# Kernel optimization log

Measured on AMD Instinct MI355X. Metric: run time of the kernel, lower is better.

Reference implementation:

```python
import jax, jax.numpy as jnp
import numpy as np

B, S, D, H, F = 8, 1024, 768, 12, 3072
DH = D // H
C_QUAD = 5.0
LN_EPS = 1e-5


def layer_norm(x, g, b):
    mu = jnp.mean(x, axis=-1, keepdims=True)
    var = jnp.mean(jnp.square(x - mu), axis=-1, keepdims=True)
    return (x - mu) * jax.lax.rsqrt(var + LN_EPS) * g + b


def setup_inputs() -> dict:
    key = jax.random.key(0)
    ks = jax.random.split(key, 8)
    s_in = 1.0 / np.sqrt(D)
    s_ff = 1.0 / np.sqrt(F)
    return {
        "x": jax.random.normal(ks[0], (B, S, D), jnp.float32),
        "wqkv": jax.random.normal(ks[1], (D, 3 * D), jnp.float32) * s_in,
        "bqkv": jnp.zeros((3 * D,), jnp.float32),
        "wo": jax.random.normal(ks[2], (D, D), jnp.float32) * s_in,
        "bo": jnp.zeros((D,), jnp.float32),
        "ln1_g": jnp.ones((D,), jnp.float32),
        "ln1_b": jnp.zeros((D,), jnp.float32),
        "w1": jax.random.normal(ks[3], (D, F), jnp.float32) * s_in,
        "b1": jnp.zeros((F,), jnp.float32),
        "w2": jax.random.normal(ks[4], (F, D), jnp.float32) * s_ff,
        "b2": jnp.zeros((D,), jnp.float32),
        "ln2_g": jnp.ones((D,), jnp.float32),
        "ln2_b": jnp.zeros((D,), jnp.float32),
    }


def quad2(scores):
    # Quad2 custom 'softmax': (s + c)^2 normalized by row sum
    s2 = jnp.square(scores + C_QUAD)
    return s2 / jnp.sum(s2, axis=-1, keepdims=True)


def reference(x, wqkv, bqkv, wo, bo, ln1_g, ln1_b, w1, b1, w2, b2, ln2_g, ln2_b):
    # --- pre-norm multi-head attention with Quad2 score normalization ---
    h = layer_norm(x, ln1_g, ln1_b)
    qkv = h @ wqkv + bqkv                              # [B,S,3D]
    q, k, v = jnp.split(qkv, 3, axis=-1)
    q = q.reshape(B, S, H, DH).transpose(0, 2, 1, 3)   # [B,H,S,Dh]
    k = k.reshape(B, S, H, DH).transpose(0, 2, 1, 3)
    v = v.reshape(B, S, H, DH).transpose(0, 2, 1, 3)
    scale = 1.0 / np.sqrt(DH)
    scores = jnp.einsum("bhqd,bhkd->bhqk", q, k) * scale
    attn = quad2(scores)                               # [B,H,S,S]
    ctx = jnp.einsum("bhqk,bhkd->bhqd", attn, v)
    ctx = ctx.transpose(0, 2, 1, 3).reshape(B, S, D)
    x = x + ctx @ wo + bo
    # --- pre-norm FFN ---
    h = layer_norm(x, ln2_g, ln2_b)
    h = jax.nn.gelu(h @ w1 + b1)
    x = x + h @ w2 + b2
    return x
```

## Files before the change

kernel.cpp:

```cpp
#include <hip/hip_runtime.h>
#include <hip/hip_bf16.h>

constexpr int B_ = 8;
constexpr int S_ = 1024;
constexpr int D_ = 768;
constexpr int H_ = 12;
constexpr int F_ = 3072;
constexpr int DH_ = 64;
constexpr int M_ = B_ * S_;
constexpr int PSZ = B_ * S_ * D_;

typedef __bf16 bf16x8 __attribute__((ext_vector_type(8)));
typedef float f32x4 __attribute__((ext_vector_type(4)));
typedef short s16x8 __attribute__((ext_vector_type(8)));
typedef short s16x4 __attribute__((ext_vector_type(4)));

__device__ __forceinline__ void gload_lds16(const __bf16* g, __bf16* l) {
    __builtin_amdgcn_global_load_lds(
        (const __attribute__((address_space(1))) void*)g,
        (__attribute__((address_space(3))) void*)l,
        16, 0, 0);
}

__device__ __forceinline__ float fast_gelu(float x) {
    float z = 0.7978845608028654f * (x + 0.044715f * x * x * x);
    z = fminf(fmaxf(z, -15.0f), 15.0f);
    float e = __builtin_amdgcn_exp2f(2.8853900817779268f * z);
    float th = (e - 1.0f) / (e + 1.0f);
    return 0.5f * x * (1.0f + th);
}

__global__ __launch_bounds__(256) void transpose_cvt(const float* __restrict__ in,
                                                     __bf16* __restrict__ out,
                                                     int K, int N) {
    __shared__ float t[32][33];
    int tx = threadIdx.x, ty = threadIdx.y;
    int n0 = blockIdx.x * 32, k0 = blockIdx.y * 32;
#pragma unroll
    for (int i = 0; i < 4; ++i)
        t[ty + i * 8][tx] = in[(size_t)(k0 + ty + i * 8) * N + n0 + tx];
    __syncthreads();
#pragma unroll
    for (int i = 0; i < 4; ++i)
        out[(size_t)(n0 + ty + i * 8) * K + k0 + tx] = (__bf16)t[tx][ty + i * 8];
}

__global__ __launch_bounds__(256) void ln_kernel(const float* __restrict__ x,
                                                 const float* __restrict__ g,
                                                 const float* __restrict__ bb,
                                                 __bf16* __restrict__ out) {
    int row = blockIdx.x;
    const float* xr = x + (size_t)row * D_;
    int tid = threadIdx.x;
    float v[3];
    float s = 0.f, s2 = 0.f;
#pragma unroll
    for (int j = 0; j < 3; ++j) {
        v[j] = xr[tid + j * 256];
        s += v[j];
        s2 += v[j] * v[j];
    }
#pragma unroll
    for (int o = 32; o >= 1; o >>= 1) {
        s += __shfl_xor(s, o, 64);
        s2 += __shfl_xor(s2, o, 64);
    }
    __shared__ float red[8];
    int wid = tid >> 6, lane = tid & 63;
    if (lane == 0) { red[wid] = s; red[4 + wid] = s2; }
    __syncthreads();
    s = red[0] + red[1] + red[2] + red[3];
    s2 = red[4] + red[5] + red[6] + red[7];
    float mu = s * (1.0f / D_);
    float var = s2 * (1.0f / D_) - mu * mu;
    float rs = rsqrtf(var + 1e-5f);
    __bf16* orow = out + (size_t)row * D_;
#pragma unroll
    for (int j = 0; j < 3; ++j) {
        int i = tid + j * 256;
        orow[i] = (__bf16)((v[j] - mu) * rs * g[i] + bb[i]);
    }
}

template <int EPI>
__global__ __launch_bounds__(256) void gemm4(const __bf16* __restrict__ A,
                                             const __bf16* __restrict__ Bt,
                                             const float* __restrict__ bias,
                                             const float* __restrict__ res,
                                             float* __restrict__ outf,
                                             __bf16* __restrict__ outb,
                                             int M, int N, int K) {
    constexpr int BK = 64;
    __shared__ __bf16 lds[2][256 * BK];

    const int tid = threadIdx.x;
    const int lane = tid & 63, wid = tid >> 6;
    const int wm = wid >> 1, wn = wid & 1;
    const int bm = blockIdx.y * 128, bn = blockIdx.x * 128;
    const int l15 = lane & 15, l4 = lane >> 4;
    f32x4 acc[4][4] = {};

    const int r8 = tid >> 3;
    const int swc = ((tid & 7) ^ (r8 & 7)) * 8;
    const __bf16* ga = A + (size_t)(bm + r8) * K + swc;
    const __bf16* gb = Bt + (size_t)(bn + r8) * K + swc;
    const int NT = K / BK;

    auto stage = [&](int t, int s) {
        const int kt = t * BK;
        __bf16* base = &lds[s][0] + tid * 8;
#pragma unroll
        for (int j = 0; j < 4; ++j)
            gload_lds16(ga + kt + (size_t)j * 32 * K, base + j * 2048);
#pragma unroll
        for (int j = 0; j < 4; ++j)
            gload_lds16(gb + kt + (size_t)j * 32 * K, base + 8192 + j * 2048);
    };

    auto compute = [&](int s) {
        const __bf16* sA = &lds[s][0];
        const __bf16* sB = &lds[s][0] + 8192;
        const int swr = (l15 & 7) * 8;
        bf16x8 a[4][2], b[4][2];
#pragma unroll
        for (int mf = 0; mf < 4; ++mf) {
            int row = wm * 64 + mf * 16 + l15;
#pragma unroll
            for (int ks = 0; ks < 2; ++ks)
                a[mf][ks] = *(const bf16x8*)&sA[row * 64 + ((ks * 32 + l4 * 8) ^ swr)];
        }
#pragma unroll
        for (int nf = 0; nf < 4; ++nf) {
            int row = wn * 64 + nf * 16 + l15;
#pragma unroll
            for (int ks = 0; ks < 2; ++ks)
                b[nf][ks] = *(const bf16x8*)&sB[row * 64 + ((ks * 32 + l4 * 8) ^ swr)];
        }
        __builtin_amdgcn_s_setprio(1);
#pragma unroll
        for (int ks = 0; ks < 2; ++ks)
#pragma unroll
            for (int mf = 0; mf < 4; ++mf)
#pragma unroll
                for (int nf = 0; nf < 4; ++nf)
                    acc[mf][nf] = __builtin_amdgcn_mfma_f32_16x16x32_bf16(
                        a[mf][ks], b[nf][ks], acc[mf][nf], 0, 0, 0);
        __builtin_amdgcn_s_setprio(0);
    };

    stage(0, 0);
    for (int t = 0; t < NT; ++t) {
        if (t + 1 < NT) {
            stage(t + 1, (t + 1) & 1);
            asm volatile("s_waitcnt vmcnt(8)" ::: "memory");
        } else {
            asm volatile("s_waitcnt vmcnt(0)" ::: "memory");
        }
        asm volatile("s_barrier" ::: "memory");
        compute(t & 1);
        asm volatile("s_barrier" ::: "memory");
    }

#pragma unroll
    for (int mf = 0; mf < 4; ++mf) {
#pragma unroll
        for (int nf = 0; nf < 4; ++nf) {
#pragma unroll
            for (int r = 0; r < 4; ++r) {
                int m = bm + wm * 64 + mf * 16 + l4 * 4 + r;
                int n = bn + wn * 64 + nf * 16 + l15;
                float val = acc[mf][nf][r] + bias[n];
                if constexpr (EPI == 0) {
                    int part = n / 768;
                    int n7 = n - part * 768;
                    int head = n7 >> 6, dh = n7 & 63;
                    int bI = m >> 10, sI = m & 1023;
                    outb[(size_t)part * PSZ +
                         (((size_t)bI * H_ + head) * S_ + sI) * DH_ + dh] = (__bf16)val;
                } else if constexpr (EPI == 1) {
                    outf[(size_t)m * N + n] = val + res[(size_t)m * N + n];
                } else {
                    outb[(size_t)m * N + n] = (__bf16)fast_gelu(val);
                }
            }
        }
    }
}

__global__ __launch_bounds__(256) void attn_kernel(const __bf16* __restrict__ qg,
                                                   const __bf16* __restrict__ kg,
                                                   const __bf16* __restrict__ vg,
                                                   __bf16* __restrict__ ctx) {
    __shared__ __bf16 Ks[64][72];
    __shared__ __bf16 Vt[64][72];
    __shared__ __bf16 Pw[4][32][72];
    __shared__ float den_l[4][32];
    int tid = threadIdx.x, lane = tid & 63, wid = tid >> 6;
    int l15 = lane & 15, l4 = lane >> 4;
    int bh = blockIdx.x >> 3, qt = blockIdx.x & 7;
    int q0 = qt * 128;
    const __bf16* qbase = qg + (size_t)bh * S_ * DH_;
    const __bf16* kbase = kg + (size_t)bh * S_ * DH_;
    const __bf16* vbase = vg + (size_t)bh * S_ * DH_;

    int wq0 = q0 + wid * 32;
    bf16x8 qf[2][2];
#pragma unroll
    for (int qi = 0; qi < 2; ++qi)
#pragma unroll
        for (int ks = 0; ks < 2; ++ks)
            qf[qi][ks] = *(const bf16x8*)(qbase + (size_t)(wq0 + qi * 16 + l15) * DH_ +
                                          ks * 32 + l4 * 8);

    f32x4 oacc[2][4] = {};
    float den[2] = {0.f, 0.f};
    const float scale = 0.125f;

    for (int k0 = 0; k0 < S_; k0 += 64) {
        {
            int key = tid >> 2, dc = (tid & 3) * 16;
            *(s16x8*)&Ks[key][dc] =
                *(const s16x8*)(kbase + (size_t)(k0 + key) * DH_ + dc);
            *(s16x8*)&Ks[key][dc + 8] =
                *(const s16x8*)(kbase + (size_t)(k0 + key) * DH_ + dc + 8);
            int vkey = tid & 63, dg = (tid >> 6) * 16;
            s16x8 v0 = *(const s16x8*)(vbase + (size_t)(k0 + vkey) * DH_ + dg);
            s16x8 v1 = *(const s16x8*)(vbase + (size_t)(k0 + vkey) * DH_ + dg + 8);
#pragma unroll
            for (int e = 0; e < 8; ++e) {
                Vt[dg + e][vkey] = ((const __bf16*)&v0)[e];
                Vt[dg + 8 + e][vkey] = ((const __bf16*)&v1)[e];
            }
        }
        __syncthreads();

        bf16x8 kf[4][2];
#pragma unroll
        for (int kfi = 0; kfi < 4; ++kfi)
#pragma unroll
            for (int ks = 0; ks < 2; ++ks)
                kf[kfi][ks] = *(const bf16x8*)&Ks[kfi * 16 + l15][ks * 32 + l4 * 8];

#pragma unroll
        for (int qi = 0; qi < 2; ++qi) {
#pragma unroll
            for (int kfi = 0; kfi < 4; ++kfi) {
                f32x4 sa = {};
                sa = __builtin_amdgcn_mfma_f32_16x16x32_bf16(kf[kfi][0], qf[qi][0], sa, 0, 0, 0);
                sa = __builtin_amdgcn_mfma_f32_16x16x32_bf16(kf[kfi][1], qf[qi][1], sa, 0, 0, 0);
                __bf16 pk[4];
#pragma unroll
                for (int r = 0; r < 4; ++r) {
                    float p = sa[r] * scale + 5.0f;
                    p = p * p;
                    den[qi] += p;
                    pk[r] = (__bf16)p;
                }
                *(s16x4*)&Pw[wid][qi * 16 + l15][kfi * 16 + l4 * 4] =
                    *(const s16x4*)pk;
            }
        }

#pragma unroll
        for (int mf = 0; mf < 2; ++mf) {
#pragma unroll
            for (int ks = 0; ks < 2; ++ks) {
                bf16x8 pa = *(const bf16x8*)&Pw[wid][mf * 16 + l15][ks * 32 + l4 * 8];
#pragma unroll
                for (int nf = 0; nf < 4; ++nf) {
                    bf16x8 vb = *(const bf16x8*)&Vt[nf * 16 + l15][ks * 32 + l4 * 8];
                    oacc[mf][nf] = __builtin_amdgcn_mfma_f32_16x16x32_bf16(
                        pa, vb, oacc[mf][nf], 0, 0, 0);
                }
            }
        }
        __syncthreads();
    }

#pragma unroll
    for (int qi = 0; qi < 2; ++qi) {
        den[qi] += __shfl_xor(den[qi], 16, 64);
        den[qi] += __shfl_xor(den[qi], 32, 64);
    }
    if (lane < 16) {
        den_l[wid][lane] = den[0];
        den_l[wid][16 + lane] = den[1];
    }
    __syncthreads();

    int b_ = bh / H_, h_ = bh - b_ * H_;
#pragma unroll
    for (int mf = 0; mf < 2; ++mf)
#pragma unroll
        for (int nf = 0; nf < 4; ++nf)
#pragma unroll
            for (int r = 0; r < 4; ++r) {
                int qrow = mf * 16 + l4 * 4 + r;
                int dcol = nf * 16 + l15;
                float val = oacc[mf][nf][r] / den_l[wid][qrow];
                int sI = q0 + wid * 32 + qrow;
                ctx[((size_t)b_ * S_ + sI) * D_ + h_ * DH_ + dcol] = (__bf16)val;
            }
}

extern "C" void kernel_launch(void* const* d_in, const int* in_sizes, int n_in,
                              void* d_out, int out_size, void* d_ws, size_t ws_size,
                              hipStream_t stream) {
    const float* x    = (const float*)d_in[0];
    const float* wqkv = (const float*)d_in[1];
    const float* bqkv = (const float*)d_in[2];
    const float* wo   = (const float*)d_in[3];
    const float* bo   = (const float*)d_in[4];
    const float* ln1g = (const float*)d_in[5];
    const float* ln1b = (const float*)d_in[6];
    const float* w1   = (const float*)d_in[7];
    const float* b1   = (const float*)d_in[8];
    const float* w2   = (const float*)d_in[9];
    const float* b2   = (const float*)d_in[10];
    const float* ln2g = (const float*)d_in[11];
    const float* ln2b = (const float*)d_in[12];
    float* out = (float*)d_out;

    char* ws = (char*)d_ws;
    size_t off = 0;
    auto alloc = [&](size_t bytes) {
        void* p = ws + off;
        off += (bytes + 255) & ~(size_t)255;
        return p;
    };
    __bf16* wqkvT = (__bf16*)alloc((size_t)(3 * D_) * D_ * 2);
    __bf16* woT   = (__bf16*)alloc((size_t)D_ * D_ * 2);
    __bf16* w1T   = (__bf16*)alloc((size_t)F_ * D_ * 2);
    __bf16* w2T   = (__bf16*)alloc((size_t)D_ * F_ * 2);
    float*  X2    = (float*)alloc((size_t)M_ * D_ * 4);
    __bf16* Hb    = (__bf16*)alloc((size_t)M_ * D_ * 2);
    __bf16* Q3    = (__bf16*)alloc((size_t)4 * PSZ * 2);
    __bf16* Kb = Q3 + (size_t)PSZ;
    __bf16* Vb = Q3 + (size_t)2 * PSZ;
    __bf16* Cx = Q3 + (size_t)3 * PSZ;

    transpose_cvt<<<dim3((3 * D_) / 32, D_ / 32), dim3(32, 8), 0, stream>>>(wqkv, wqkvT, D_, 3 * D_);
    transpose_cvt<<<dim3(D_ / 32, D_ / 32), dim3(32, 8), 0, stream>>>(wo, woT, D_, D_);
    transpose_cvt<<<dim3(F_ / 32, D_ / 32), dim3(32, 8), 0, stream>>>(w1, w1T, D_, F_);
    transpose_cvt<<<dim3(D_ / 32, F_ / 32), dim3(32, 8), 0, stream>>>(w2, w2T, F_, D_);

    ln_kernel<<<M_, 256, 0, stream>>>(x, ln1g, ln1b, Hb);
    gemm4<0><<<dim3((3 * D_) / 128, M_ / 128), 256, 0, stream>>>(
        Hb, wqkvT, bqkv, nullptr, nullptr, Q3, M_, 3 * D_, D_);
    attn_kernel<<<B_ * H_ * (S_ / 128), 256, 0, stream>>>(Q3, Kb, Vb, Cx);
    gemm4<1><<<dim3(D_ / 128, M_ / 128), 256, 0, stream>>>(
        Cx, woT, bo, x, X2, nullptr, M_, D_, D_);
    ln_kernel<<<M_, 256, 0, stream>>>(X2, ln2g, ln2b, Hb);
    gemm4<2><<<dim3(F_ / 128, M_ / 128), 256, 0, stream>>>(
        Hb, w1T, b1, nullptr, nullptr, Q3, M_, F_, D_);
    gemm4<1><<<dim3(D_ / 128, M_ / 128), 256, 0, stream>>>(
        Q3, w2T, b2, X2, out, nullptr, M_, D_, F_);
    (void)in_sizes; (void)n_in; (void)out_size; (void)ws_size;
}
```

Measured before the change: 255.3 us.

## Use 256x256 tile GEMM with 512 threads for QKV and FFN1

Adds a gemm256 kernel with 256x256 output tiles, 8 waves and 128 KB of double-buffered LDS, and uses it for the QKV projection and the first FFN GEMM. Larger tiles raise arithmetic intensity and cut global reloads of A and B. In exchange each block holds more accumulator registers and LDS, so occupancy drops. The grid also shrinks, to 288 blocks for QKV and 384 for FFN1, which may underfill the GPU's CUs and cause wave-quantization loss. It adds s_setprio around the MFMA bursts.

```diff
diff --git a/kernel.cpp b/kernel.cpp
--- a/kernel.cpp
+++ b/kernel.cpp
@@ -83,6 +83,112 @@
 }
 
 template <int EPI>
+__global__ __launch_bounds__(512, 2) void gemm256(const __bf16* __restrict__ A,
+                                                  const __bf16* __restrict__ Bt,
+                                                  const float* __restrict__ bias,
+                                                  float* __restrict__ outf,
+                                                  __bf16* __restrict__ outb,
+                                                  int M, int N, int K) {
+    __shared__ __bf16 lds[2][32768];
+
+    const int tid = threadIdx.x;
+    const int lane = tid & 63, wid = tid >> 6;
+    const int wm = wid >> 2, wn = wid & 3;
+    const int bm = blockIdx.y * 256, bn = blockIdx.x * 256;
+    const int l15 = lane & 15, l4 = lane >> 4;
+    f32x4 acc[8][4] = {};
+
+    const int r8 = tid >> 3;
+    const int swc = ((tid & 7) ^ (r8 & 7)) * 8;
+    const __bf16* ga = A + (size_t)(bm + r8) * K + swc;
+    const __bf16* gb = Bt + (size_t)(bn + r8) * K + swc;
+    const int NT = K / 64;
+
+    auto stage = [&](int t, int s) {
+        const int kt = t * 64;
+        __bf16* base = &lds[s][0] + tid * 8;
+#pragma unroll
+        for (int j = 0; j < 4; ++j)
+            gload_lds16(ga + kt + (size_t)j * 64 * K, base + j * 4096);
+#pragma unroll
+        for (int j = 0; j < 4; ++j)
+            gload_lds16(gb + kt + (size_t)j * 64 * K, base + 16384 + j * 4096);
+    };
+
+    auto compute = [&](int s) {
+        const __bf16* sA = &lds[s][0];
+        const __bf16* sB = &lds[s][0] + 16384;
+        const int swr = (l15 & 7) * 8;
+        bf16x8 b[4][2];
+#pragma unroll
+        for (int nf = 0; nf < 4; ++nf) {
+            int row = wn * 64 + nf * 16 + l15;
+#pragma unroll
+            for (int ks = 0; ks < 2; ++ks)
+                b[nf][ks] = *(const bf16x8*)&sB[row * 64 + ((ks * 32 + l4 * 8) ^ swr)];
+        }
+#pragma unroll
+        for (int half = 0; half < 2; ++half) {
+            bf16x8 a[4][2];
+#pragma unroll
+            for (int mi = 0; mi < 4; ++mi) {
+                int row = wm * 128 + half * 64 + mi * 16 + l15;
+#pragma unroll
+                for (int ks = 0; ks < 2; ++ks)
+                    a[mi][ks] = *(const bf16x8*)&sA[row * 64 + ((ks * 32 + l4 * 8) ^ swr)];
+            }
+            __builtin_amdgcn_s_setprio(1);
+#pragma unroll
+            for (int ks = 0; ks < 2; ++ks)
+#pragma unroll
+                for (int mi = 0; mi < 4; ++mi)
+#pragma unroll
+                    for (int nf = 0; nf < 4; ++nf)
+                        acc[half * 4 + mi][nf] = __builtin_amdgcn_mfma_f32_16x16x32_bf16(
+                            a[mi][ks], b[nf][ks], acc[half * 4 + mi][nf], 0, 0, 0);
+            __builtin_amdgcn_s_setprio(0);
+        }
+    };
+
+    stage(0, 0);
+    for (int t = 0; t < NT; ++t) {
+        if (t + 1 < NT) {
+            stage(t + 1, (t + 1) & 1);
+            asm volatile("s_waitcnt vmcnt(8)" ::: "memory");
+        } else {
+            asm volatile("s_waitcnt vmcnt(0)" ::: "memory");
+        }
+        asm volatile("s_barrier" ::: "memory");
+        compute(t & 1);
+        asm volatile("s_barrier" ::: "memory");
+    }
+
+#pragma unroll
+    for (int mf = 0; mf < 8; ++mf) {
+#pragma unroll
+        for (int nf = 0; nf < 4; ++nf) {
+#pragma unroll
+            for (int r = 0; r < 4; ++r) {
+                int m = bm + wm * 128 + mf * 16 + l4 * 4 + r;
+                int n = bn + wn * 64 + nf * 16 + l15;
+                float val = acc[mf][nf][r] + bias[n];
+                if constexpr (EPI == 0) {
+                    int part = n / 768;
+                    int n7 = n - part * 768;
+                    int head = n7 >> 6, dh = n7 & 63;
+                    int bI = m >> 10, sI = m & 1023;
+                    outb[(size_t)part * PSZ +
+                         (((size_t)bI * H_ + head) * S_ + sI) * DH_ + dh] = (__bf16)val;
+                } else {
+                    outb[(size_t)m * N + n] = (__bf16)fast_gelu(val);
+                }
+            }
+        }
+    }
+    (void)outf;
+}
+
+template <int EPI>
 __global__ __launch_bounds__(256) void gemm4(const __bf16* __restrict__ A,
                                              const __bf16* __restrict__ Bt,
                                              const float* __restrict__ bias,
@@ -170,14 +276,7 @@
                 int m = bm + wm * 64 + mf * 16 + l4 * 4 + r;
                 int n = bn + wn * 64 + nf * 16 + l15;
                 float val = acc[mf][nf][r] + bias[n];
-                if constexpr (EPI == 0) {
-                    int part = n / 768;
-                    int n7 = n - part * 768;
-                    int head = n7 >> 6, dh = n7 & 63;
-                    int bI = m >> 10, sI = m & 1023;
-                    outb[(size_t)part * PSZ +
-                         (((size_t)bI * H_ + head) * S_ + sI) * DH_ + dh] = (__bf16)val;
-                } else if constexpr (EPI == 1) {
+                if constexpr (EPI == 1) {
                     outf[(size_t)m * N + n] = val + res[(size_t)m * N + n];
                 } else {
                     outb[(size_t)m * N + n] = (__bf16)fast_gelu(val);
@@ -345,14 +444,14 @@
     transpose_cvt<<<dim3(D_ / 32, F_ / 32), dim3(32, 8), 0, stream>>>(w2, w2T, F_, D_);
 
     ln_kernel<<<M_, 256, 0, stream>>>(x, ln1g, ln1b, Hb);
-    gemm4<0><<<dim3((3 * D_) / 128, M_ / 128), 256, 0, stream>>>(
-        Hb, wqkvT, bqkv, nullptr, nullptr, Q3, M_, 3 * D_, D_);
+    gemm256<0><<<dim3((3 * D_) / 256, M_ / 256), 512, 0, stream>>>(
+        Hb, wqkvT, bqkv, nullptr, Q3, M_, 3 * D_, D_);
     attn_kernel<<<B_ * H_ * (S_ / 128), 256, 0, stream>>>(Q3, Kb, Vb, Cx);
     gemm4<1><<<dim3(D_ / 128, M_ / 128), 256, 0, stream>>>(
         Cx, woT, bo, x, X2, nullptr, M_, D_, D_);
     ln_kernel<<<M_, 256, 0, stream>>>(X2, ln2g, ln2b, Hb);
-    gemm4<2><<<dim3(F_ / 128, M_ / 128), 256, 0, stream>>>(
-        Hb, w1T, b1, nullptr, nullptr, Q3, M_, F_, D_);
+    gemm256<2><<<dim3(F_ / 256, M_ / 256), 512, 0, stream>>>(
+        Hb, w1T, b1, nullptr, Q3, M_, F_, D_);
     gemm4<1><<<dim3(D_ / 128, M_ / 128), 256, 0, stream>>>(
         Q3, w2T, b2, X2, out, nullptr, M_, D_, F_);
     (void)in_sizes; (void)n_in; (void)out_size; (void)ws_size;
```

New measurement: 288.7 us. +13.1%, slower.
